# Kernel tuning notes

Hardware: AMD Instinct MI355X
Metric: run time of the kernel (lower is better)

## Reference

```python
import jax, jax.numpy as jnp
import numpy as np

VOXEL_SIZE = 32


def setup_inputs() -> dict:
    key = jax.random.key(0)
    k1, k2 = jax.random.split(key)
    B, N, F = 16, 8192, 256
    local_features = jax.random.normal(k1, (B, N, F), dtype=jnp.float32)
    # is_norm=False path: coords are used directly as normalized [0,1] values
    keypoint_coords = jax.random.uniform(k2, (B, N, 2), dtype=jnp.float32)
    return {"local_features": local_features, "keypoint_coords": keypoint_coords}


def _flat_indices(keypoint_coords, batch_size, voxel_size):
    # normalize_and_quantize with is_norm=False: use coords directly
    gx = jnp.clip((keypoint_coords[..., 0] * (voxel_size - 1)).astype(jnp.int32), 0, voxel_size - 1)
    gy = jnp.clip((keypoint_coords[..., 1] * (voxel_size - 1)).astype(jnp.int32), 0, voxel_size - 1)
    # flat index = gy*V + gx + b*V*V, matching the torch flat view layout
    batch_off = jnp.arange(batch_size, dtype=jnp.int32)[:, None] * (voxel_size * voxel_size)
    return (gy * voxel_size + gx + batch_off).reshape(-1)  # [B*N]


def reference(local_features, keypoint_coords):
    V = VOXEL_SIZE
    B, N, F = local_features.shape
    idx = _flat_indices(keypoint_coords, B, V)  # [B*N]
    num_seg = B * V * V
    flat_feat = local_features.reshape(B * N, F)
    # scatter_reduce amax with include_self=False: untouched cells keep initial 0
    seg_max = jax.ops.segment_max(flat_feat, idx, num_segments=num_seg)  # [B*V*V, F]
    counts = jax.ops.segment_sum(jnp.ones((B * N,), jnp.float32), idx, num_segments=num_seg)
    voxel_grid = jnp.where(counts[:, None] > 0, seg_max, jnp.zeros((), flat_feat.dtype))
    return voxel_grid.reshape(B, V, V, F)
```

## Files before the change

### kernel.cpp

```cpp
#include <hip/hip_runtime.h>
#include <math.h>

#define VOXEL 32
#define CAP 64
#define OVF_MAX 4096


__device__ __forceinline__ int cell_of(const float* __restrict__ coords, int point, int N) {
    float x = coords[(size_t)point * 2 + 0];
    float y = coords[(size_t)point * 2 + 1];
    int gx = (int)(x * (float)(VOXEL - 1));
    int gy = (int)(y * (float)(VOXEL - 1));
    gx = min(max(gx, 0), VOXEL - 1);
    gy = min(max(gy, 0), VOXEL - 1);
    int b = point / N;
    return b * (VOXEL * VOXEL) + gy * VOXEL + gx;
}


__global__ void zero_kernel(unsigned int* __restrict__ p, int n) {
    int i = blockIdx.x * blockDim.x + threadIdx.x;
    if (i < n) p[i] = 0u;
}

__global__ void scatter_bucket(const float* __restrict__ coords,
                               unsigned int* __restrict__ counts,
                               unsigned int* __restrict__ sorted,
                               unsigned int* __restrict__ ovf_cnt,
                               unsigned int* __restrict__ ovf_list,
                               int BN, int N) {
    int p = blockIdx.x * blockDim.x + threadIdx.x;
    if (p >= BN) return;
    int c = cell_of(coords, p, N);
    unsigned int pos = atomicAdd(&counts[c], 1u);
    if (pos < CAP) {
        sorted[(size_t)c * CAP + pos] = (unsigned int)p;
    } else {
        unsigned int o = atomicAdd(ovf_cnt, 1u);
        if (o < OVF_MAX) ovf_list[o] = (unsigned int)p;
    }
}

__global__ void gather_kernel(const float* __restrict__ feat,
                              const unsigned int* __restrict__ sorted,
                              const unsigned int* __restrict__ counts,
                              float* __restrict__ out) {
    const int wave = threadIdx.x >> 6;
    const int lane = threadIdx.x & 63;
    const int cell = blockIdx.x * 4 + wave;

    const unsigned int cnt = min(counts[cell], (unsigned int)CAP);

    float4 m = make_float4(-INFINITY, -INFINITY, -INFINITY, -INFINITY);
    const unsigned int base = (unsigned int)cell * CAP;
    unsigned int pid_l = (lane < (int)cnt) ? sorted[base + lane] : 0u;
    for (unsigned int j = 0; j < cnt; ++j) {
        const unsigned int pid = (unsigned int)__shfl((int)pid_l, (int)j);
        const float4 v = *(const float4*)(feat + (size_t)pid * 256 + lane * 4);
        m.x = fmaxf(m.x, v.x);
        m.y = fmaxf(m.y, v.y);
        m.z = fmaxf(m.z, v.z);
        m.w = fmaxf(m.w, v.w);
    }
    if (cnt == 0) m = make_float4(0.f, 0.f, 0.f, 0.f);
    *(float4*)(out + (size_t)cell * 256 + lane * 4) = m;
}

__global__ void cleanup_kernel(const float* __restrict__ feat,
                               const float* __restrict__ coords,
                               const unsigned int* __restrict__ ovf_cnt,
                               const unsigned int* __restrict__ ovf_list,
                               float* __restrict__ out, int N) {
    unsigned int n = min(*ovf_cnt, (unsigned int)OVF_MAX);
    if (n == 0) return;
    const int wave = threadIdx.x >> 6;
    const int lane = threadIdx.x & 63;
    for (unsigned int i = wave; i < n; i += 4) {
        unsigned int p = ovf_list[i];
        int c = cell_of(coords, p, N);
#pragma unroll
        for (int k = 0; k < 4; ++k) {
            float v = feat[(size_t)p * 256 + lane * 4 + k];
            unsigned int* addr = (unsigned int*)&out[(size_t)c * 256 + lane * 4 + k];
            float old = __uint_as_float(*addr);
            while (v > old) {
                unsigned int assumed = __float_as_uint(old);
                unsigned int prev = atomicCAS(addr, assumed, __float_as_uint(v));
                if (prev == assumed) break;
                old = __uint_as_float(prev);
            }
        }
    }
}


__device__ __forceinline__ unsigned int enc_f32(float f) {
    unsigned int u = __float_as_uint(f);
    return (u & 0x80000000u) ? ~u : (u | 0x80000000u);
}
__device__ __forceinline__ float dec_f32(unsigned int u) {
    return __uint_as_float((u & 0x80000000u) ? (u ^ 0x80000000u) : ~u);
}

__global__ void voxel_scatter_max(const float* __restrict__ feat,
                                  const float* __restrict__ coords,
                                  unsigned int* __restrict__ out,
                                  int BN, int N, int F) {
    int gid   = blockIdx.x * blockDim.x + threadIdx.x;
    int point = gid / (F / 4);
    int fi    = gid % (F / 4);
    if (point >= BN) return;
    int idx = cell_of(coords, point, N);
    const float4 v = *(const float4*)(feat + (size_t)point * F + fi * 4);
    unsigned int* o = out + (size_t)idx * F + fi * 4;
    atomicMax(o + 0, enc_f32(v.x));
    atomicMax(o + 1, enc_f32(v.y));
    atomicMax(o + 2, enc_f32(v.z));
    atomicMax(o + 3, enc_f32(v.w));
}

__global__ void voxel_decode(unsigned int* __restrict__ out, int n4) {
    int i = blockIdx.x * blockDim.x + threadIdx.x;
    if (i >= n4) return;
    uint4 u = ((const uint4*)out)[i];
    float4 f;
    f.x = (u.x == 0u) ? 0.0f : dec_f32(u.x);
    f.y = (u.y == 0u) ? 0.0f : dec_f32(u.y);
    f.z = (u.z == 0u) ? 0.0f : dec_f32(u.z);
    f.w = (u.w == 0u) ? 0.0f : dec_f32(u.w);
    ((float4*)out)[i] = f;
}


extern "C" void kernel_launch(void* const* d_in, const int* in_sizes, int n_in,
                              void* d_out, int out_size, void* d_ws, size_t ws_size,
                              hipStream_t stream) {
    const float* feat   = (const float*)d_in[0];
    const float* coords = (const float*)d_in[1];

    const int BN = in_sizes[1] / 2;
    const int F  = in_sizes[0] / BN;
    const int B  = out_size / (VOXEL * VOXEL * F);
    const int N  = BN / B;
    const int ncells = B * VOXEL * VOXEL;

    const size_t ws_need = ((size_t)ncells + 16 + OVF_MAX + (size_t)ncells * CAP) * 4;
    const bool fast_ok = (F == 256) && (ncells == 16384) && ((BN & (N - 1)) == 0) &&
                         (ws_size >= ws_need);

    if (fast_ok) {
        unsigned int* counts   = (unsigned int*)d_ws;
        unsigned int* ovf_cnt  = counts + ncells;
        unsigned int* ovf_list = ovf_cnt + 16;
        unsigned int* sorted   = ovf_list + OVF_MAX;

        const int nzero = ncells + 16;
        zero_kernel<<<(nzero + 255) / 256, 256, 0, stream>>>(counts, nzero);
        scatter_bucket<<<(BN + 255) / 256, 256, 0, stream>>>(coords, counts, sorted,
                                                             ovf_cnt, ovf_list, BN, N);
        gather_kernel<<<ncells / 4, 256, 0, stream>>>(feat, sorted, counts, (float*)d_out);
        cleanup_kernel<<<1, 256, 0, stream>>>(feat, coords, ovf_cnt, ovf_list,
                                              (float*)d_out, N);
    } else {
        unsigned int* out = (unsigned int*)d_out;
        hipMemsetAsync(d_out, 0, (size_t)out_size * sizeof(float), stream);
        int threads = BN * (F / 4);
        voxel_scatter_max<<<(threads + 255) / 256, 256, 0, stream>>>(feat, coords, out, BN, N, F);
        int n4 = out_size / 4;
        voxel_decode<<<(n4 + 255) / 256, 256, 0, stream>>>(out, n4);
    }
}
```

Measured before the change: 42.10 us.

## Unroll gather loads by eight and fold overflow cleanup into gather kernel

The gather loop now issues eight independent feature loads per iteration, with clamped shuffle indices, so more memory requests are in flight per wave. The separate single-block cleanup kernel, which used CAS atomics for points past the bucket capacity, is removed. Instead each wave scans the overflow list and merges the points that fall in its cell, which saves a launch and the serial cleanup pass. The cost is redundant loads when the count is not a multiple of eight, and an O(overflow) scan per cell whenever overflow happens.

```diff
diff --git a/kernel.cpp b/kernel.cpp
--- a/kernel.cpp
+++ b/kernel.cpp
@@ -2,6 +2,7 @@
 #include <math.h>
 
 #define VOXEL 32
+#define NCELL (VOXEL * VOXEL)
 #define CAP 64
 #define OVF_MAX 4096
 
@@ -14,7 +15,12 @@
     gx = min(max(gx, 0), VOXEL - 1);
     gy = min(max(gy, 0), VOXEL - 1);
     int b = point / N;
-    return b * (VOXEL * VOXEL) + gy * VOXEL + gx;
+    return b * NCELL + gy * VOXEL + gx;
+}
+
+__device__ __forceinline__ void fmax4(float4& m, const float4 v) {
+    m.x = fmaxf(m.x, v.x); m.y = fmaxf(m.y, v.y);
+    m.z = fmaxf(m.z, v.z); m.w = fmaxf(m.w, v.w);
 }
 
 
@@ -31,7 +37,12 @@
                                int BN, int N) {
     int p = blockIdx.x * blockDim.x + threadIdx.x;
     if (p >= BN) return;
-    int c = cell_of(coords, p, N);
+    const float2 xy = ((const float2*)coords)[p];
+    int gx = (int)(xy.x * (float)(VOXEL - 1));
+    int gy = (int)(xy.y * (float)(VOXEL - 1));
+    gx = min(max(gx, 0), VOXEL - 1);
+    gy = min(max(gy, 0), VOXEL - 1);
+    int c = (p / N) * NCELL + gy * VOXEL + gx;
     unsigned int pos = atomicAdd(&counts[c], 1u);
     if (pos < CAP) {
         sorted[(size_t)c * CAP + pos] = (unsigned int)p;
@@ -41,56 +52,60 @@
     }
 }
 
-__global__ void gather_kernel(const float* __restrict__ feat,
-                              const unsigned int* __restrict__ sorted,
-                              const unsigned int* __restrict__ counts,
-                              float* __restrict__ out) {
+__global__ void __launch_bounds__(256)
+gather_kernel(const float* __restrict__ feat,
+              const float* __restrict__ coords,
+              const unsigned int* __restrict__ sorted,
+              const unsigned int* __restrict__ counts,
+              const unsigned int* __restrict__ ovf_cnt,
+              const unsigned int* __restrict__ ovf_list,
+              float* __restrict__ out, int N, int F) {
     const int wave = threadIdx.x >> 6;
     const int lane = threadIdx.x & 63;
     const int cell = blockIdx.x * 4 + wave;
 
-    const unsigned int cnt = min(counts[cell], (unsigned int)CAP);
+    const unsigned int raw = counts[cell];
+    const int cnt = (int)min(raw, (unsigned int)CAP);
+    const size_t cb = (size_t)cell * CAP;
+    unsigned int pid_l = (lane < cnt) ? sorted[cb + lane] : 0u;
 
     float4 m = make_float4(-INFINITY, -INFINITY, -INFINITY, -INFINITY);
-    const unsigned int base = (unsigned int)cell * CAP;
-    unsigned int pid_l = (lane < (int)cnt) ? sorted[base + lane] : 0u;
-    for (unsigned int j = 0; j < cnt; ++j) {
-        const unsigned int pid = (unsigned int)__shfl((int)pid_l, (int)j);
-        const float4 v = *(const float4*)(feat + (size_t)pid * 256 + lane * 4);
-        m.x = fmaxf(m.x, v.x);
-        m.y = fmaxf(m.y, v.y);
-        m.z = fmaxf(m.z, v.z);
-        m.w = fmaxf(m.w, v.w);
+    const int e = cnt - 1;
+    for (int j = 0; j < cnt; j += 8) {
+        const int p0 = __shfl((int)pid_l, min(j + 0, e));
+        const int p1 = __shfl((int)pid_l, min(j + 1, e));
+        const int p2 = __shfl((int)pid_l, min(j + 2, e));
+        const int p3 = __shfl((int)pid_l, min(j + 3, e));
+        const int p4 = __shfl((int)pid_l, min(j + 4, e));
+        const int p5 = __shfl((int)pid_l, min(j + 5, e));
+        const int p6 = __shfl((int)pid_l, min(j + 6, e));
+        const int p7 = __shfl((int)pid_l, min(j + 7, e));
+        const float4 v0 = *(const float4*)(feat + (size_t)p0 * F + lane * 4);
+        const float4 v1 = *(const float4*)(feat + (size_t)p1 * F + lane * 4);
+        const float4 v2 = *(const float4*)(feat + (size_t)p2 * F + lane * 4);
+        const float4 v3 = *(const float4*)(feat + (size_t)p3 * F + lane * 4);
+        const float4 v4 = *(const float4*)(feat + (size_t)p4 * F + lane * 4);
+        const float4 v5 = *(const float4*)(feat + (size_t)p5 * F + lane * 4);
+        const float4 v6 = *(const float4*)(feat + (size_t)p6 * F + lane * 4);
+        const float4 v7 = *(const float4*)(feat + (size_t)p7 * F + lane * 4);
+        fmax4(m, v0); fmax4(m, v1); fmax4(m, v2); fmax4(m, v3);
+        fmax4(m, v4); fmax4(m, v5); fmax4(m, v6); fmax4(m, v7);
     }
-    if (cnt == 0) m = make_float4(0.f, 0.f, 0.f, 0.f);
-    *(float4*)(out + (size_t)cell * 256 + lane * 4) = m;
-}
 
-__global__ void cleanup_kernel(const float* __restrict__ feat,
-                               const float* __restrict__ coords,
-                               const unsigned int* __restrict__ ovf_cnt,
-                               const unsigned int* __restrict__ ovf_list,
-                               float* __restrict__ out, int N) {
-    unsigned int n = min(*ovf_cnt, (unsigned int)OVF_MAX);
-    if (n == 0) return;
-    const int wave = threadIdx.x >> 6;
-    const int lane = threadIdx.x & 63;
-    for (unsigned int i = wave; i < n; i += 4) {
-        unsigned int p = ovf_list[i];
-        int c = cell_of(coords, p, N);
-#pragma unroll
-        for (int k = 0; k < 4; ++k) {
-            float v = feat[(size_t)p * 256 + lane * 4 + k];
-            unsigned int* addr = (unsigned int*)&out[(size_t)c * 256 + lane * 4 + k];
-            float old = __uint_as_float(*addr);
-            while (v > old) {
-                unsigned int assumed = __float_as_uint(old);
-                unsigned int prev = atomicCAS(addr, assumed, __float_as_uint(v));
-                if (prev == assumed) break;
-                old = __uint_as_float(prev);
+    const unsigned int novf = *ovf_cnt;
+    if (novf != 0u) {
+        const int n = (int)min(novf, (unsigned int)OVF_MAX);
+        for (int i = 0; i < n; ++i) {
+            const unsigned int p = ovf_list[i];
+            if (cell_of(coords, (int)p, N) == cell) {
+                const float4 v = *(const float4*)(feat + (size_t)p * F + lane * 4);
+                fmax4(m, v);
             }
         }
     }
+
+    if (raw == 0u) m = make_float4(0.f, 0.f, 0.f, 0.f);
+    *(float4*)(out + (size_t)cell * F + lane * 4) = m;
 }
 
 
@@ -99,6 +114,7 @@
     return (u & 0x80000000u) ? ~u : (u | 0x80000000u);
 }
 __device__ __forceinline__ float dec_f32(unsigned int u) {
+    if (u == 0u) return 0.0f;
     return __uint_as_float((u & 0x80000000u) ? (u ^ 0x80000000u) : ~u);
 }
 
@@ -124,10 +140,8 @@
     if (i >= n4) return;
     uint4 u = ((const uint4*)out)[i];
     float4 f;
-    f.x = (u.x == 0u) ? 0.0f : dec_f32(u.x);
-    f.y = (u.y == 0u) ? 0.0f : dec_f32(u.y);
-    f.z = (u.z == 0u) ? 0.0f : dec_f32(u.z);
-    f.w = (u.w == 0u) ? 0.0f : dec_f32(u.w);
+    f.x = dec_f32(u.x); f.y = dec_f32(u.y);
+    f.z = dec_f32(u.z); f.w = dec_f32(u.w);
     ((float4*)out)[i] = f;
 }
 
@@ -137,36 +151,36 @@
                               hipStream_t stream) {
     const float* feat   = (const float*)d_in[0];
     const float* coords = (const float*)d_in[1];
+    float* out          = (float*)d_out;
 
     const int BN = in_sizes[1] / 2;
     const int F  = in_sizes[0] / BN;
-    const int B  = out_size / (VOXEL * VOXEL * F);
+    const int B  = out_size / (NCELL * F);
     const int N  = BN / B;
-    const int ncells = B * VOXEL * VOXEL;
+    const int totc = B * NCELL;
 
-    const size_t ws_need = ((size_t)ncells + 16 + OVF_MAX + (size_t)ncells * CAP) * 4;
-    const bool fast_ok = (F == 256) && (ncells == 16384) && ((BN & (N - 1)) == 0) &&
+    const size_t ws_need = ((size_t)totc + 16 + OVF_MAX + (size_t)totc * CAP) * 4;
+    const bool fast_ok = (F == 256) && (B * N == BN) && (B * NCELL * F == out_size) &&
                          (ws_size >= ws_need);
 
     if (fast_ok) {
         unsigned int* counts   = (unsigned int*)d_ws;
-        unsigned int* ovf_cnt  = counts + ncells;
+        unsigned int* ovf_cnt  = counts + totc;
         unsigned int* ovf_list = ovf_cnt + 16;
         unsigned int* sorted   = ovf_list + OVF_MAX;
 
-        const int nzero = ncells + 16;
-        zero_kernel<<<(nzero + 255) / 256, 256, 0, stream>>>(counts, nzero);
+        zero_kernel<<<(totc + 16 + 255) / 256, 256, 0, stream>>>(counts, totc + 16);
         scatter_bucket<<<(BN + 255) / 256, 256, 0, stream>>>(coords, counts, sorted,
                                                              ovf_cnt, ovf_list, BN, N);
-        gather_kernel<<<ncells / 4, 256, 0, stream>>>(feat, sorted, counts, (float*)d_out);
-        cleanup_kernel<<<1, 256, 0, stream>>>(feat, coords, ovf_cnt, ovf_list,
-                                              (float*)d_out, N);
+        gather_kernel<<<totc / 4, 256, 0, stream>>>(feat, coords, sorted, counts,
+                                                    ovf_cnt, ovf_list, out, N, F);
     } else {
-        unsigned int* out = (unsigned int*)d_out;
         hipMemsetAsync(d_out, 0, (size_t)out_size * sizeof(float), stream);
         int threads = BN * (F / 4);
-        voxel_scatter_max<<<(threads + 255) / 256, 256, 0, stream>>>(feat, coords, out, BN, N, F);
+        voxel_scatter_max<<<(threads + 255) / 256, 256, 0, stream>>>(feat, coords,
+                                                                     (unsigned int*)d_out,
+                                                                     BN, N, F);
         int n4 = out_size / 4;
-        voxel_decode<<<(n4 + 255) / 256, 256, 0, stream>>>(out, n4);
+        voxel_decode<<<(n4 + 255) / 256, 256, 0, stream>>>((unsigned int*)d_out, n4);
     }
 }
```

After: 39.53 us. 1.07x faster.
